# Optimization experiments

Measured on AMD Instinct MI355X. Metric: run time of the kernel, lower is better.

## Reference

```python
import jax, jax.numpy as jnp
import numpy as np

B, T, FC, FX = 64, 1024, 256, 512

def setup_inputs() -> dict:
    key = jax.random.key(0)
    kC, kX, kW, kb = jax.random.split(key, 4)
    C = jax.random.normal(kC, (B, T, FC), dtype=jnp.float32)
    X = jax.random.normal(kX, (B, T, FX), dtype=jnp.float32)
    # nn.Linear(encoding_size, context_size): W [fc, fx], b [fc]
    lim = 1.0 / np.sqrt(FX)
    W = jax.random.uniform(kW, (FC, FX), minval=-lim, maxval=lim, dtype=jnp.float32)
    b = jax.random.uniform(kb, (FC,), minval=-lim, maxval=lim, dtype=jnp.float32)
    return {"C": C, "X": X, "W": W, "b": b}

def reference(C, X, W, b):
    # Xt = Linear(X): [B, T, fc]
    Xt = jnp.einsum('btx,cx->btc', X, W) + b
    # Z[i, j, t] = <C[i, t, :], Xt[j, t, :]>  -> per-timestep BxB similarity
    Z = jnp.einsum('itc,jtc->ijt', C, Xt)
    # logsumexp over the negatives axis (dim 1), numerically stable
    lse = jax.nn.logsumexp(Z, axis=1)          # [B, T]
    Zdiag = jnp.einsum('iit->it', Z)           # [B, T], Z[i, i, t]
    return jnp.mean(Zdiag - lse)
```

## Files before the change

### kernel.cpp

```cpp
#include <hip/hip_runtime.h>

#define B_  64
#define T_  1024
#define FC_ 256
#define FX_ 512

typedef __bf16 bf16x8 __attribute__((ext_vector_type(8)));
typedef float  f32x4  __attribute__((ext_vector_type(4)));

__device__ __forceinline__ unsigned short f2bf(float f) {
  union { float f; unsigned int u; } v; v.f = f;
  unsigned int r = v.u + 0x7fffu + ((v.u >> 16) & 1u);
  return (unsigned short)(r >> 16);
}
__device__ __forceinline__ unsigned int pk2(float lo, float hi) {
  return (unsigned int)f2bf(lo) | ((unsigned int)f2bf(hi) << 16);
}
__device__ __forceinline__ uint4 pk8(float4 a, float4 b) {
  uint4 p;
  p.x = pk2(a.x, a.y); p.y = pk2(a.z, a.w);
  p.z = pk2(b.x, b.y); p.w = pk2(b.z, b.w);
  return p;
}

__global__ void k_wcvt(const float* __restrict__ W, unsigned short* __restrict__ Wb,
                       float* __restrict__ out) {
  const int i = blockIdx.x * 256 + threadIdx.x;
  float4 v = ((const float4*)W)[i];
  ushort4 h;
  h.x = f2bf(v.x); h.y = f2bf(v.y); h.z = f2bf(v.z); h.w = f2bf(v.w);
  ((ushort4*)Wb)[i] = h;
  if (i == 0) out[0] = 0.f;
}

__global__ __launch_bounds__(256, 4)
void k_fused(const float* __restrict__ C, const float* __restrict__ X,
             const unsigned short* __restrict__ Wb, const float* __restrict__ bias,
             float* __restrict__ out)
{
  __shared__ __align__(16) char sMem[40960];
  char* sX  = sMem;
  char* sXt = sMem + 8192;

  const int t    = blockIdx.x;
  const int tid  = threadIdx.x;
  const int lane = tid & 63;
  const int wid  = tid >> 6;
  const int l15  = lane & 15;
  const int lhi  = lane >> 4;

  const int xrow = tid >> 2;
  const int xcb  = (tid & 3) * 32;
  const float* xptr = X + ((size_t)xrow * T_ + t) * FX_ + ((tid & 3) << 4);
  const int xwbase = xrow * 128;
  const int xsw    = (xrow & 7) << 4;

  const char* wbase = (const char*)Wb + (size_t)(wid * 64 + l15) * 1024 + lhi * 16;

  float bv[4];
  #pragma unroll
  for (int n2 = 0; n2 < 4; ++n2) bv[n2] = bias[wid * 64 + n2 * 16 + l15];

  float4 xb[4];
  {
    float4 xa[4];
    #pragma unroll
    for (int q = 0; q < 4; ++q) xa[q] = *(const float4*)(xptr + q * 4);
    #pragma unroll
    for (int q = 0; q < 4; ++q) xb[q] = *(const float4*)(xptr + 64 + q * 4);
    uint4 p0 = pk8(xa[0], xa[1]);
    uint4 p1 = pk8(xa[2], xa[3]);
    *(uint4*)(sX + xwbase + ((xcb +  0) ^ xsw)) = p0;
    *(uint4*)(sX + xwbase + ((xcb + 16) ^ xsw)) = p1;
  }

  f32x4 acc[4][4];
  #pragma unroll
  for (int i = 0; i < 4; ++i)
    #pragma unroll
    for (int n2 = 0; n2 < 4; ++n2)
      #pragma unroll
      for (int r = 0; r < 4; ++r) acc[i][n2][r] = 0.f;

  __syncthreads();

  #pragma unroll
  for (int k = 0; k < 8; ++k) {
    #pragma unroll
    for (int kk = 0; kk < 2; ++kk) {
      bf16x8 afr[4];
      #pragma unroll
      for (int i = 0; i < 4; ++i) {
        const int ar = i * 16 + l15;
        afr[i] = *(const bf16x8*)(sX + ar * 128 + ((kk * 64 + lhi * 16) ^ ((ar & 7) << 4)));
      }
      #pragma unroll
      for (int n2 = 0; n2 < 4; ++n2) {
        bf16x8 w = *(const bf16x8*)(wbase + n2 * 16384 + k * 128 + kk * 64);
        #pragma unroll
        for (int i = 0; i < 4; ++i)
          acc[i][n2] = __builtin_amdgcn_mfma_f32_16x16x32_bf16(afr[i], w, acc[i][n2], 0, 0, 0);
      }
    }
    __syncthreads();
    if (k < 7) {
      float4 xn[4];
      if (k < 6) {
        #pragma unroll
        for (int q = 0; q < 4; ++q) xn[q] = *(const float4*)(xptr + (k + 2) * 64 + q * 4);
      }
      uint4 p0 = pk8(xb[0], xb[1]);
      uint4 p1 = pk8(xb[2], xb[3]);
      *(uint4*)(sX + xwbase + ((xcb +  0) ^ xsw)) = p0;
      *(uint4*)(sX + xwbase + ((xcb + 16) ^ xsw)) = p1;
      __syncthreads();
      if (k < 6) {
        #pragma unroll
        for (int q = 0; q < 4; ++q) xb[q] = xn[q];
      }
    }
  }

  const float* cptr = C + ((size_t)(wid * 16 + l15) * T_ + t) * FC_ + lhi * 8;
  float4 cv[8];
  #pragma unroll
  for (int q = 0; q < 4; ++q) {
    cv[2 * q]     = *(const float4*)(cptr + q * 32);
    cv[2 * q + 1] = *(const float4*)(cptr + q * 32 + 4);
  }

  #pragma unroll
  for (int i = 0; i < 4; ++i)
    #pragma unroll
    for (int n2 = 0; n2 < 4; ++n2) {
      const int c2 = (wid * 64 + n2 * 16 + l15) * 2;
      #pragma unroll
      for (int r = 0; r < 4; ++r) {
        const int j = i * 16 + lhi * 4 + r;
        *(unsigned short*)(sXt + j * 512 + (c2 ^ ((j & 7) << 4))) =
            f2bf(acc[i][n2][r] + bv[n2]);
      }
    }

  bf16x8 ca[4];
  #pragma unroll
  for (int q = 0; q < 4; ++q) ca[q] = __builtin_bit_cast(bf16x8, pk8(cv[2 * q], cv[2 * q + 1]));
  float4 cw[8];
  #pragma unroll
  for (int q = 0; q < 4; ++q) {
    cw[2 * q]     = *(const float4*)(cptr + 128 + q * 32);
    cw[2 * q + 1] = *(const float4*)(cptr + 128 + q * 32 + 4);
  }
  __syncthreads();

  f32x4 z[4];
  #pragma unroll
  for (int n = 0; n < 4; ++n)
    #pragma unroll
    for (int r = 0; r < 4; ++r) z[n][r] = 0.f;

  #pragma unroll
  for (int q = 0; q < 4; ++q) {
    #pragma unroll
    for (int n = 0; n < 4; ++n) {
      const int br = n * 16 + l15;
      bf16x8 b = *(const bf16x8*)(sXt + br * 512 + ((q * 64 + lhi * 16) ^ ((br & 7) << 4)));
      z[n] = __builtin_amdgcn_mfma_f32_16x16x32_bf16(ca[q], b, z[n], 0, 0, 0);
    }
  }
  #pragma unroll
  for (int q = 0; q < 4; ++q) ca[q] = __builtin_bit_cast(bf16x8, pk8(cw[2 * q], cw[2 * q + 1]));
  #pragma unroll
  for (int q = 0; q < 4; ++q) {
    #pragma unroll
    for (int n = 0; n < 4; ++n) {
      const int br = n * 16 + l15;
      bf16x8 b = *(const bf16x8*)(sXt + br * 512 + (((q + 4) * 64 + lhi * 16) ^ ((br & 7) << 4)));
      z[n] = __builtin_amdgcn_mfma_f32_16x16x32_bf16(ca[q], b, z[n], 0, 0, 0);
    }
  }

  float partial = 0.f;
  #pragma unroll
  for (int r = 0; r < 4; ++r) {
    float m = fmaxf(fmaxf(z[0][r], z[1][r]), fmaxf(z[2][r], z[3][r]));
    #pragma unroll
    for (int d = 1; d < 16; d <<= 1) m = fmaxf(m, __shfl_xor(m, d));
    float s = __expf(z[0][r] - m) + __expf(z[1][r] - m) +
              __expf(z[2][r] - m) + __expf(z[3][r] - m);
    #pragma unroll
    for (int d = 1; d < 16; d <<= 1) s += __shfl_xor(s, d);
    const float lse = m + __logf(s);
    float dv = 0.f;
    #pragma unroll
    for (int n = 0; n < 4; ++n) dv = (n == wid) ? z[n][r] : dv;
    if (l15 == lhi * 4 + r) partial += dv - lse;
  }
  #pragma unroll
  for (int d = 1; d < 64; d <<= 1) partial += __shfl_xor(partial, d);
  if (lane == 0) atomicAdd(out, partial * (1.0f / (B_ * T_)));
}

extern "C" void kernel_launch(void* const* d_in, const int* in_sizes, int n_in,
                              void* d_out, int out_size, void* d_ws, size_t ws_size,
                              hipStream_t stream) {
  const float* C  = (const float*)d_in[0];
  const float* X  = (const float*)d_in[1];
  const float* W  = (const float*)d_in[2];
  const float* bb = (const float*)d_in[3];
  unsigned short* Wb = (unsigned short*)d_ws;
  float* out = (float*)d_out;

  k_wcvt <<<dim3(128),  dim3(256), 0, stream>>>(W, Wb, out);
  k_fused<<<dim3(1024), dim3(256), 0, stream>>>(C, X, Wb, bb, out);
}
```

Measured before the change: 297.5 us.

## Use 512-thread blocks, stage full X tile in LDS, prefetch W registers

Each block now has 8 waves instead of 4, each computing 32 output columns of the linear projection. The whole 64x512 bf16 X tile is loaded into shared memory at once, which removes the per-chunk double-buffer sync loop, and W fragments are software-prefetched one step ahead. Only 4 waves run the similarity/logsumexp stage, and the Xt buffer now reuses the X region. Shared memory grows to 64KB per block, which lowers occupancy, and half the waves idle during the second GEMM.

```diff
diff --git a/kernel.cpp b/kernel.cpp
--- a/kernel.cpp
+++ b/kernel.cpp
@@ -33,14 +33,14 @@
   if (i == 0) out[0] = 0.f;
 }
 
-__global__ __launch_bounds__(256, 4)
+__global__ __launch_bounds__(512, 4)
 void k_fused(const float* __restrict__ C, const float* __restrict__ X,
              const unsigned short* __restrict__ Wb, const float* __restrict__ bias,
              float* __restrict__ out)
 {
-  __shared__ __align__(16) char sMem[40960];
+  __shared__ __align__(16) char sMem[65536];
   char* sX  = sMem;
-  char* sXt = sMem + 8192;
+  char* sXt = sMem;
 
   const int t    = blockIdx.x;
   const int tid  = threadIdx.x;
@@ -49,156 +49,124 @@
   const int l15  = lane & 15;
   const int lhi  = lane >> 4;
 
-  const int xrow = tid >> 2;
-  const int xcb  = (tid & 3) * 32;
-  const float* xptr = X + ((size_t)xrow * T_ + t) * FX_ + ((tid & 3) << 4);
-  const int xwbase = xrow * 128;
-  const int xsw    = (xrow & 7) << 4;
+  const int xrow = tid >> 3;
+  const int xg   = tid & 7;
+  const float* xptr = X + ((size_t)xrow * T_ + t) * FX_ + xg * 8;
 
-  const char* wbase = (const char*)Wb + (size_t)(wid * 64 + l15) * 1024 + lhi * 16;
-
-  float bv[4];
+  float4 xv[16];
   #pragma unroll
-  for (int n2 = 0; n2 < 4; ++n2) bv[n2] = bias[wid * 64 + n2 * 16 + l15];
-
-  float4 xb[4];
-  {
-    float4 xa[4];
-    #pragma unroll
-    for (int q = 0; q < 4; ++q) xa[q] = *(const float4*)(xptr + q * 4);
-    #pragma unroll
-    for (int q = 0; q < 4; ++q) xb[q] = *(const float4*)(xptr + 64 + q * 4);
-    uint4 p0 = pk8(xa[0], xa[1]);
-    uint4 p1 = pk8(xa[2], xa[3]);
-    *(uint4*)(sX + xwbase + ((xcb +  0) ^ xsw)) = p0;
-    *(uint4*)(sX + xwbase + ((xcb + 16) ^ xsw)) = p1;
+  for (int q = 0; q < 8; ++q) {
+    xv[2 * q]     = *(const float4*)(xptr + 64 * q);
+    xv[2 * q + 1] = *(const float4*)(xptr + 64 * q + 4);
   }
 
-  f32x4 acc[4][4];
+  const float bv0 = bias[wid * 32 + l15];
+  const float bv1 = bias[wid * 32 + 16 + l15];
+
+  f32x4 acc[4][2];
   #pragma unroll
   for (int i = 0; i < 4; ++i)
     #pragma unroll
-    for (int n2 = 0; n2 < 4; ++n2)
+    for (int n2 = 0; n2 < 2; ++n2)
       #pragma unroll
       for (int r = 0; r < 4; ++r) acc[i][n2][r] = 0.f;
 
+  const int xswz = (xrow & 7) << 4;
+  #pragma unroll
+  for (int q = 0; q < 8; ++q) {
+    *(uint4*)(sX + xrow * 1024 + ((xg * 16 + 128 * q) ^ xswz)) =
+        pk8(xv[2 * q], xv[2 * q + 1]);
+  }
   __syncthreads();
 
+  const char* wrow = (const char*)Wb + (size_t)(wid * 32 + l15) * 1024 + lhi * 16;
+  bf16x8 wc0 = *(const bf16x8*)(wrow);
+  bf16x8 wc1 = *(const bf16x8*)(wrow + 16384);
   #pragma unroll
-  for (int k = 0; k < 8; ++k) {
+  for (int s = 0; s < 16; ++s) {
+    bf16x8 wn0, wn1;
+    if (s < 15) {
+      wn0 = *(const bf16x8*)(wrow + (s + 1) * 64);
+      wn1 = *(const bf16x8*)(wrow + 16384 + (s + 1) * 64);
+    }
+    bf16x8 afr[4];
     #pragma unroll
-    for (int kk = 0; kk < 2; ++kk) {
-      bf16x8 afr[4];
-      #pragma unroll
-      for (int i = 0; i < 4; ++i) {
-        const int ar = i * 16 + l15;
-        afr[i] = *(const bf16x8*)(sX + ar * 128 + ((kk * 64 + lhi * 16) ^ ((ar & 7) << 4)));
-      }
-      #pragma unroll
-      for (int n2 = 0; n2 < 4; ++n2) {
-        bf16x8 w = *(const bf16x8*)(wbase + n2 * 16384 + k * 128 + kk * 64);
-        #pragma unroll
-        for (int i = 0; i < 4; ++i)
-          acc[i][n2] = __builtin_amdgcn_mfma_f32_16x16x32_bf16(afr[i], w, acc[i][n2], 0, 0, 0);
-      }
+    for (int i = 0; i < 4; ++i) {
+      const int ar = i * 16 + l15;
+      afr[i] = *(const bf16x8*)(sX + ar * 1024 + ((s * 64 + lhi * 16) ^ ((ar & 7) << 4)));
     }
-    __syncthreads();
-    if (k < 7) {
-      float4 xn[4];
-      if (k < 6) {
-        #pragma unroll
-        for (int q = 0; q < 4; ++q) xn[q] = *(const float4*)(xptr + (k + 2) * 64 + q * 4);
-      }
-      uint4 p0 = pk8(xb[0], xb[1]);
-      uint4 p1 = pk8(xb[2], xb[3]);
-      *(uint4*)(sX + xwbase + ((xcb +  0) ^ xsw)) = p0;
-      *(uint4*)(sX + xwbase + ((xcb + 16) ^ xsw)) = p1;
-      __syncthreads();
-      if (k < 6) {
-        #pragma unroll
-        for (int q = 0; q < 4; ++q) xb[q] = xn[q];
-      }
+    #pragma unroll
+    for (int i = 0; i < 4; ++i) {
+      acc[i][0] = __builtin_amdgcn_mfma_f32_16x16x32_bf16(afr[i], wc0, acc[i][0], 0, 0, 0);
+      acc[i][1] = __builtin_amdgcn_mfma_f32_16x16x32_bf16(afr[i], wc1, acc[i][1], 0, 0, 0);
+    }
+    if (s < 15) { wc0 = wn0; wc1 = wn1; }
+  }
+  __syncthreads();
+
+  float4 cv[16];
+  if (wid < 4) {
+    const float* cptr = C + ((size_t)(wid * 16 + l15) * T_ + t) * FC_ + lhi * 8;
+    #pragma unroll
+    for (int s = 0; s < 8; ++s) {
+      cv[2 * s]     = *(const float4*)(cptr + 32 * s);
+      cv[2 * s + 1] = *(const float4*)(cptr + 32 * s + 4);
     }
   }
 
-  const float* cptr = C + ((size_t)(wid * 16 + l15) * T_ + t) * FC_ + lhi * 8;
-  float4 cv[8];
-  #pragma unroll
-  for (int q = 0; q < 4; ++q) {
-    cv[2 * q]     = *(const float4*)(cptr + q * 32);
-    cv[2 * q + 1] = *(const float4*)(cptr + q * 32 + 4);
-  }
-
-  #pragma unroll
-  for (int i = 0; i < 4; ++i)
+  {
+    const int c0 = (wid * 32 + l15) * 2;
+    const int c1 = (wid * 32 + 16 + l15) * 2;
     #pragma unroll
-    for (int n2 = 0; n2 < 4; ++n2) {
-      const int c2 = (wid * 64 + n2 * 16 + l15) * 2;
+    for (int i = 0; i < 4; ++i)
       #pragma unroll
       for (int r = 0; r < 4; ++r) {
-        const int j = i * 16 + lhi * 4 + r;
-        *(unsigned short*)(sXt + j * 512 + (c2 ^ ((j & 7) << 4))) =
-            f2bf(acc[i][n2][r] + bv[n2]);
+        const int j   = i * 16 + lhi * 4 + r;
+        const int rsw = (j & 7) << 4;
+        *(unsigned short*)(sXt + j * 512 + (c0 ^ rsw)) = f2bf(acc[i][0][r] + bv0);
+        *(unsigned short*)(sXt + j * 512 + (c1 ^ rsw)) = f2bf(acc[i][1][r] + bv1);
+      }
+  }
+  __syncthreads();
+
+  if (wid < 4) {
+    f32x4 z[4];
+    #pragma unroll
+    for (int n = 0; n < 4; ++n)
+      #pragma unroll
+      for (int r = 0; r < 4; ++r) z[n][r] = 0.f;
+
+    #pragma unroll
+    for (int s = 0; s < 8; ++s) {
+      bf16x8 ca = __builtin_bit_cast(bf16x8, pk8(cv[2 * s], cv[2 * s + 1]));
+      #pragma unroll
+      for (int n = 0; n < 4; ++n) {
+        const int br = n * 16 + l15;
+        bf16x8 b = *(const bf16x8*)(sXt + br * 512 + ((s * 64 + lhi * 16) ^ ((br & 7) << 4)));
+        z[n] = __builtin_amdgcn_mfma_f32_16x16x32_bf16(ca, b, z[n], 0, 0, 0);
       }
     }
 
-  bf16x8 ca[4];
-  #pragma unroll
-  for (int q = 0; q < 4; ++q) ca[q] = __builtin_bit_cast(bf16x8, pk8(cv[2 * q], cv[2 * q + 1]));
-  float4 cw[8];
-  #pragma unroll
-  for (int q = 0; q < 4; ++q) {
-    cw[2 * q]     = *(const float4*)(cptr + 128 + q * 32);
-    cw[2 * q + 1] = *(const float4*)(cptr + 128 + q * 32 + 4);
+    float partial = 0.f;
+    #pragma unroll
+    for (int r = 0; r < 4; ++r) {
+      float m = fmaxf(fmaxf(z[0][r], z[1][r]), fmaxf(z[2][r], z[3][r]));
+      #pragma unroll
+      for (int d = 1; d < 16; d <<= 1) m = fmaxf(m, __shfl_xor(m, d));
+      float s = __expf(z[0][r] - m) + __expf(z[1][r] - m) +
+                __expf(z[2][r] - m) + __expf(z[3][r] - m);
+      #pragma unroll
+      for (int d = 1; d < 16; d <<= 1) s += __shfl_xor(s, d);
+      const float lse = m + __logf(s);
+      float dv = 0.f;
+      #pragma unroll
+      for (int n = 0; n < 4; ++n) dv = (n == wid) ? z[n][r] : dv;
+      if (l15 == lhi * 4 + r) partial += dv - lse;
+    }
+    #pragma unroll
+    for (int d = 1; d < 64; d <<= 1) partial += __shfl_xor(partial, d);
+    if (lane == 0) atomicAdd(out, partial * (1.0f / (B_ * T_)));
   }
-  __syncthreads();
-
-  f32x4 z[4];
-  #pragma unroll
-  for (int n = 0; n < 4; ++n)
-    #pragma unroll
-    for (int r = 0; r < 4; ++r) z[n][r] = 0.f;
-
-  #pragma unroll
-  for (int q = 0; q < 4; ++q) {
-    #pragma unroll
-    for (int n = 0; n < 4; ++n) {
-      const int br = n * 16 + l15;
-      bf16x8 b = *(const bf16x8*)(sXt + br * 512 + ((q * 64 + lhi * 16) ^ ((br & 7) << 4)));
-      z[n] = __builtin_amdgcn_mfma_f32_16x16x32_bf16(ca[q], b, z[n], 0, 0, 0);
-    }
-  }
-  #pragma unroll
-  for (int q = 0; q < 4; ++q) ca[q] = __builtin_bit_cast(bf16x8, pk8(cw[2 * q], cw[2 * q + 1]));
-  #pragma unroll
-  for (int q = 0; q < 4; ++q) {
-    #pragma unroll
-    for (int n = 0; n < 4; ++n) {
-      const int br = n * 16 + l15;
-      bf16x8 b = *(const bf16x8*)(sXt + br * 512 + (((q + 4) * 64 + lhi * 16) ^ ((br & 7) << 4)));
-      z[n] = __builtin_amdgcn_mfma_f32_16x16x32_bf16(ca[q], b, z[n], 0, 0, 0);
-    }
-  }
-
-  float partial = 0.f;
-  #pragma unroll
-  for (int r = 0; r < 4; ++r) {
-    float m = fmaxf(fmaxf(z[0][r], z[1][r]), fmaxf(z[2][r], z[3][r]));
-    #pragma unroll
-    for (int d = 1; d < 16; d <<= 1) m = fmaxf(m, __shfl_xor(m, d));
-    float s = __expf(z[0][r] - m) + __expf(z[1][r] - m) +
-              __expf(z[2][r] - m) + __expf(z[3][r] - m);
-    #pragma unroll
-    for (int d = 1; d < 16; d <<= 1) s += __shfl_xor(s, d);
-    const float lse = m + __logf(s);
-    float dv = 0.f;
-    #pragma unroll
-    for (int n = 0; n < 4; ++n) dv = (n == wid) ? z[n][r] : dv;
-    if (l15 == lhi * 4 + r) partial += dv - lse;
-  }
-  #pragma unroll
-  for (int d = 1; d < 64; d <<= 1) partial += __shfl_xor(partial, d);
-  if (lane == 0) atomicAdd(out, partial * (1.0f / (B_ * T_)));
 }
 
 extern "C" void kernel_launch(void* const* d_in, const int* in_sizes, int n_in,
@@ -212,5 +180,5 @@
   float* out = (float*)d_out;
 
   k_wcvt <<<dim3(128),  dim3(256), 0, stream>>>(W, Wb, out);
-  k_fused<<<dim3(1024), dim3(256), 0, stream>>>(C, X, Wb, bb, out);
+  k_fused<<<dim3(1024), dim3(512), 0, stream>>>(C, X, Wb, bb, out);
 }
```

New measurement: 269.4 us. 1.1x faster.
